# Kernel optimization log

Hardware: AMD Instinct MI355X
Metric: run time of the kernel (lower is better)

Reference implementation:

```python
import jax, jax.numpy as jnp
import numpy as np

N = 100000      # nodes
E = 800000      # directed edges
D_IN = 128      # input features (n_inputs)
HIDDEN = 128    # conf['model']['hidden_size']
D_OUT = 2       # conv2 output classes


def setup_inputs() -> dict:
    key = jax.random.key(0)
    k0, k1, k2, k3 = jax.random.split(key, 4)
    x = jax.random.normal(k0, (N, D_IN), dtype=jnp.float32)
    edge_index = jax.random.randint(k1, (2, E), 0, N, dtype=jnp.int32)
    # Glorot-style init for GCNConv weights, zero bias (PyG defaults)
    s1 = float(np.sqrt(6.0 / (D_IN + HIDDEN)))
    s2 = float(np.sqrt(6.0 / (HIDDEN + D_OUT)))
    W1 = jax.random.uniform(k2, (D_IN, HIDDEN), jnp.float32, -s1, s1)
    b1 = jnp.zeros((HIDDEN,), jnp.float32)
    W2 = jax.random.uniform(k3, (HIDDEN, D_OUT), jnp.float32, -s2, s2)
    b2 = jnp.zeros((D_OUT,), jnp.float32)
    return {"x": x, "edge_index": edge_index, "W1": W1, "b1": b1, "W2": W2, "b2": b2}


def gcn_conv(x, src, dst, W, b):
    """PyG GCNConv: add self-loops, symmetric deg^-1/2 A deg^-1/2 normalization."""
    n = x.shape[0]
    h = x @ W                                                   # [N, F_out]
    ones_e = jnp.ones((src.shape[0],), h.dtype)
    # degree with self-loops (init to 1)
    deg = jnp.ones((n,), h.dtype).at[dst].add(ones_e)           # [N]
    dinv = 1.0 / jnp.sqrt(deg)
    norm = (dinv[src] * dinv[dst])[:, None]                     # [E, 1]
    # self-loop contribution: norm_ii = dinv_i^2; then scatter edge messages
    out = (h * (dinv * dinv)[:, None]).at[dst].add(h[src] * norm)
    return out + b


def reference(x, edge_index, W1, b1, W2, b2):
    src, dst = edge_index[0], edge_index[1]
    h = jax.nn.relu(gcn_conv(x, src, dst, W1, b1))
    return gcn_conv(h, src, dst, W2, b2)                        # [N, 2]
```

## Files before the change

kernel.cpp:

```cpp
#include <hip/hip_runtime.h>
#include <hip/hip_bf16.h>


#define D1 128
#define BSH 8
#define BSZ (1 << BSH)
#define NBMAX 1024
#define CHA 2048
#define BMM 128

typedef __attribute__((ext_vector_type(8))) short short8;
typedef __attribute__((ext_vector_type(4))) float floatx4;

__device__ __forceinline__ unsigned short f2bf(float f) {
    unsigned u = __float_as_uint(f);
    u += 0x7fff + ((u >> 16) & 1);
    return (unsigned short)(u >> 16);
}
__device__ __forceinline__ float bflo(unsigned u) { return __uint_as_float(u << 16); }
__device__ __forceinline__ float bfhi(unsigned u) { return __uint_as_float(u & 0xffff0000u); }
__device__ __forceinline__ int clampN(int s, int N) {
    return (int)min((unsigned)s, (unsigned)N);
}

__global__ void k_init(const float* __restrict__ W1, unsigned short* __restrict__ W1t,
                       int* __restrict__ bcur, unsigned short* __restrict__ h1s,
                       float* __restrict__ h2s, float* __restrict__ dinv, int N) {
    int i = blockIdx.x * 256 + threadIdx.x;
    if (i < NBMAX) bcur[i] = 0;
    if (i < D1) h1s[(size_t)N * D1 + i] = 0;
    if (i < 2)  h2s[(size_t)N * 2 + i] = 0.f;
    if (i == 0) dinv[N] = 0.f;
    if (i < D1 * D1) {
        int c = i >> 7, k = i & 127;
        W1t[c * D1 + k] = f2bf(W1[k * D1 + c]);
    }
}

__global__ __launch_bounds__(512) void k_gemm1_binA(
    const float* __restrict__ x, const unsigned short* __restrict__ W1t,
    unsigned short* __restrict__ h1s,
    const int* __restrict__ src, const int* __restrict__ dst,
    int* __restrict__ bcur, unsigned* __restrict__ packed,
    int N, int E, int nbuck, int CAP, int GA, int GG)
{
    __shared__ __align__(16) char smem[2 * BMM * 136 * 2];

    const int b = blockIdx.x;
    const int m2 = 2 * min(GA, GG);
    bool isA;
    int bid;
    if (b < m2)            { isA = (b & 1); bid = b >> 1; }
    else if (GA <= GG)     { isA = false;   bid = min(GA, GG) + (b - m2); }
    else                   { isA = true;    bid = min(GA, GG) + (b - m2); }

    if (isA) {
        int* hist = (int*)smem;
        int* cur  = hist + NBMAX;
        const int t = threadIdx.x;
        const int e0 = bid * CHA;
        const int e1 = min(e0 + CHA, E);

        for (int i = t; i < nbuck; i += 512) hist[i] = 0;
        __syncthreads();
        for (int i = e0 + t; i < e1; i += 512)
            atomicAdd(&hist[dst[i] >> BSH], 1);
        __syncthreads();
        for (int i = t; i < nbuck; i += 512)
            cur[i] = (hist[i] > 0) ? atomicAdd(&bcur[i], hist[i]) : 0;
        __syncthreads();
        for (int i = e0 + t; i < e1; i += 512) {
            int d = dst[i];
            int bk = d >> BSH;
            int pos = atomicAdd(&cur[bk], 1);
            if (pos < CAP)
                packed[(size_t)bk * CAP + pos] =
                    ((unsigned)src[i] << BSH) | (unsigned)(d & (BSZ - 1));
        }
        return;
    }

    unsigned short (*Xs)[136] = (unsigned short(*)[136])smem;
    unsigned short (*Ws)[136] = (unsigned short(*)[136])(smem + BMM * 136 * 2);

    const int t = threadIdx.x;
    const int row0 = bid * BMM;

#pragma unroll
    for (int i = 0; i < 4; ++i) {
        int idx = t + 512 * i;
        int r = idx >> 4, c8 = idx & 15;
        short8 v = ((const short8*)W1t)[r * 16 + c8];
        *(short8*)&Ws[r][c8 * 8] = v;
    }
#pragma unroll
    for (int i = 0; i < 4; ++i) {
        int idx = t + 512 * i;
        int r = idx >> 4, c8 = idx & 15;
        int row = row0 + r;
        short8 v8 = (short8)0;
        if (row < N) {
            const float* p = x + (size_t)row * D1 + c8 * 8;
            float4 f0 = *(const float4*)p;
            float4 f1 = *(const float4*)(p + 4);
            v8[0] = (short)f2bf(f0.x); v8[1] = (short)f2bf(f0.y);
            v8[2] = (short)f2bf(f0.z); v8[3] = (short)f2bf(f0.w);
            v8[4] = (short)f2bf(f1.x); v8[5] = (short)f2bf(f1.y);
            v8[6] = (short)f2bf(f1.z); v8[7] = (short)f2bf(f1.w);
        }
        *(short8*)&Xs[r][c8 * 8] = v8;
    }
    __syncthreads();

    const int w = t >> 6;
    const int l = t & 63;
    const int m = l & 15;
    const int q = l >> 4;

    floatx4 acc[8];
#pragma unroll
    for (int c = 0; c < 8; ++c) acc[c] = (floatx4)0.0f;

#pragma unroll
    for (int ks = 0; ks < 4; ++ks) {
        short8 a = *(const short8*)&Xs[16 * w + m][ks * 32 + q * 8];
#pragma unroll
        for (int c = 0; c < 8; ++c) {
            short8 bb = *(const short8*)&Ws[c * 16 + m][ks * 32 + q * 8];
            acc[c] = __builtin_amdgcn_mfma_f32_16x16x32_bf16(a, bb, acc[c], 0, 0, 0);
        }
    }

    __syncthreads();

#pragma unroll
    for (int r = 0; r < 4; ++r) {
        int rt = 16 * w + q * 4 + r;
#pragma unroll
        for (int c = 0; c < 8; ++c)
            Xs[rt][c * 16 + m] = f2bf(acc[c][r]);
    }
    __syncthreads();

#pragma unroll
    for (int i = 0; i < 4; ++i) {
        int idx = t + 512 * i;
        int r = idx >> 4, c8 = idx & 15;
        int row = row0 + r;
        if (row < N)
            *(short8*)&h1s[(size_t)row * D1 + c8 * 8] = *(const short8*)&Xs[r][c8 * 8];
    }
}

__global__ __launch_bounds__(BSZ) void k_binB(
    const int* __restrict__ bcur, const unsigned* __restrict__ packed,
    int2* __restrict__ rp, float* __restrict__ dinv,
    int* __restrict__ esrc, int* __restrict__ order, int N, int CAP)
{
    __shared__ int lh[BSZ];
    __shared__ int lcur[BSZ];
    __shared__ int wsum[BSZ / 64];
    __shared__ int dbin[64];
    __shared__ int dcur[64];

    const int t = threadIdx.x;
    const int s = blockIdx.x << BSH;
    const int n = min(BSZ, N - s);
    const int base = blockIdx.x * CAP;
    const int cnt = min(bcur[blockIdx.x], CAP);

    lh[t] = 0;
    if (t < 64) dbin[t] = 0;
    __syncthreads();
    for (int i = t; i < cnt; i += BSZ)
        atomicAdd(&lh[packed[base + i] & (BSZ - 1)], 1);
    __syncthreads();

    const int deg = lh[t];
    const int pdeg = (deg + 3) & ~3;

    int inc = pdeg;
#pragma unroll
    for (int off = 1; off < 64; off <<= 1) {
        int u = __shfl_up(inc, off);
        if ((t & 63) >= off) inc += u;
    }
    if ((t & 63) == 63) wsum[t >> 6] = inc;
    __syncthreads();
    if (t < BSZ / 64) {
        int w = wsum[t];
#pragma unroll
        for (int off = 1; off < BSZ / 64; off <<= 1) {
            int u = __shfl_up(w, off, BSZ / 64);
            if ((t & (BSZ / 64 - 1)) >= off) w += u;
        }
        wsum[t] = w;
    }
    __syncthreads();
    int excl = ((t >> 6) ? wsum[(t >> 6) - 1] : 0) + inc - pdeg;

    if (t < n) {
        rp[s + t] = make_int2(base + excl, deg);
        dinv[s + t] = rsqrtf(1.0f + (float)deg);
        atomicAdd(&dbin[63 - min(deg, 63)], 1);
        for (int k = deg; k < pdeg; ++k) {
            int p = excl + k;
            if (p < CAP) esrc[base + p] = N;
        }
    }
    lcur[t] = excl;
    __syncthreads();

    for (int i = t; i < cnt; i += BSZ) {
        unsigned p = packed[base + i];
        int ld = (int)(p & (BSZ - 1));
        int pos = atomicAdd(&lcur[ld], 1);
        if (pos < CAP) esrc[base + pos] = (int)(p >> BSH);
    }

    __syncthreads();
    if (t < 64) {
        int dv = dbin[t];
        int dinc = dv;
#pragma unroll
        for (int off = 1; off < 64; off <<= 1) {
            int u = __shfl_up(dinc, off);
            if (t >= off) dinc += u;
        }
        dcur[t] = dinc - dv;
    }
    __syncthreads();
    if (t < n) {
        int b = 63 - min(deg, 63);
        int pos = atomicAdd(&dcur[b], 1);
        order[s + pos] = s + t;
    }
}

#define ACC8F(A, v, d) \
    A[0] += bflo(v.x) * d; A[1] += bfhi(v.x) * d; \
    A[2] += bflo(v.y) * d; A[3] += bfhi(v.y) * d; \
    A[4] += bflo(v.z) * d; A[5] += bfhi(v.z) * d; \
    A[6] += bflo(v.w) * d; A[7] += bfhi(v.w) * d;

__global__ __launch_bounds__(256) void k_agg1_gemm2(
    const int2* __restrict__ rp, const int* __restrict__ esrc,
    const int* __restrict__ order,
    const float* __restrict__ dinv, const unsigned short* __restrict__ h1s,
    const float* __restrict__ b1, const float* __restrict__ W2,
    float* __restrict__ h2s, int N)
{
    int gid = blockIdx.x * 256 + threadIdx.x;
    int grp = gid >> 4;
    if (grp >= N) return;
    int node = order[grp];
    int lane = gid & 15;

    const uint4* h1v = (const uint4*)h1s;
    const int4*  ev  = (const int4*)esrc;

    float di = dinv[node];
    uint4 u = h1v[(size_t)node * 16 + lane];
    float accA[8], accB[8];
    accA[0] = bflo(u.x) * di; accA[1] = bfhi(u.x) * di;
    accA[2] = bflo(u.y) * di; accA[3] = bfhi(u.y) * di;
    accA[4] = bflo(u.z) * di; accA[5] = bfhi(u.z) * di;
    accA[6] = bflo(u.w) * di; accA[7] = bfhi(u.w) * di;
#pragma unroll
    for (int j = 0; j < 8; ++j) accB[j] = 0.f;

    int2 r = rp[node];
    int beg = r.x;
    int end4 = beg + ((r.y + 3) & ~3);

    for (int e = beg; e < end4; e += 8) {
        int q = e >> 2;
        int4 i0 = ev[q];
        int4 i1 = ev[q + 1];
        bool c1 = (e + 4) < end4;
        int s0 = clampN(i0.x, N), s1 = clampN(i0.y, N);
        int s2 = clampN(i0.z, N), s3 = clampN(i0.w, N);
        int s4 = c1 ? clampN(i1.x, N) : N, s5 = c1 ? clampN(i1.y, N) : N;
        int s6 = c1 ? clampN(i1.z, N) : N, s7 = c1 ? clampN(i1.w, N) : N;
        float d0 = dinv[s0], d1 = dinv[s1], d2 = dinv[s2], d3 = dinv[s3];
        float d4 = dinv[s4], d5 = dinv[s5], d6 = dinv[s6], d7 = dinv[s7];
        uint4 v0 = h1v[(size_t)s0 * 16 + lane];
        uint4 v1 = h1v[(size_t)s1 * 16 + lane];
        uint4 v2 = h1v[(size_t)s2 * 16 + lane];
        uint4 v3 = h1v[(size_t)s3 * 16 + lane];
        uint4 v4 = h1v[(size_t)s4 * 16 + lane];
        uint4 v5 = h1v[(size_t)s5 * 16 + lane];
        uint4 v6 = h1v[(size_t)s6 * 16 + lane];
        uint4 v7 = h1v[(size_t)s7 * 16 + lane];
        ACC8F(accA, v0, d0) ACC8F(accB, v1, d1) ACC8F(accA, v2, d2) ACC8F(accB, v3, d3)
        ACC8F(accA, v4, d4) ACC8F(accB, v5, d5) ACC8F(accA, v6, d6) ACC8F(accB, v7, d7)
    }

    const float4* b1v = (const float4*)b1;
    float4 bbA = b1v[lane * 2 + 0];
    float4 bbB = b1v[lane * 2 + 1];
    float a[8];
    a[0] = fmaxf((accA[0] + accB[0]) * di + bbA.x, 0.f);
    a[1] = fmaxf((accA[1] + accB[1]) * di + bbA.y, 0.f);
    a[2] = fmaxf((accA[2] + accB[2]) * di + bbA.z, 0.f);
    a[3] = fmaxf((accA[3] + accB[3]) * di + bbA.w, 0.f);
    a[4] = fmaxf((accA[4] + accB[4]) * di + bbB.x, 0.f);
    a[5] = fmaxf((accA[5] + accB[5]) * di + bbB.y, 0.f);
    a[6] = fmaxf((accA[6] + accB[6]) * di + bbB.z, 0.f);
    a[7] = fmaxf((accA[7] + accB[7]) * di + bbB.w, 0.f);

    const float4* W2v = (const float4*)W2;
    float p0 = 0.f, p1 = 0.f;
#pragma unroll
    for (int j2 = 0; j2 < 4; ++j2) {
        float4 wv = W2v[lane * 4 + j2];
        p0 += a[j2 * 2] * wv.x + a[j2 * 2 + 1] * wv.z;
        p1 += a[j2 * 2] * wv.y + a[j2 * 2 + 1] * wv.w;
    }

#pragma unroll
    for (int off = 8; off > 0; off >>= 1) {
        p0 += __shfl_xor(p0, off);
        p1 += __shfl_xor(p1, off);
    }
    if (lane == 0) {
        h2s[(size_t)node * 2 + 0] = p0 * di;
        h2s[(size_t)node * 2 + 1] = p1 * di;
    }
}

__global__ void k_gather2(const int2* __restrict__ rp, const int* __restrict__ esrc,
                          const float* __restrict__ h2s, const float* __restrict__ dinv,
                          const float* __restrict__ b2, float* __restrict__ out, int N)
{
    int i = blockIdx.x * 256 + threadIdx.x;
    if (i >= N) return;
    const float2* h2v = (const float2*)h2s;
    const int4* ev = (const int4*)esrc;
    float2 h = h2v[i];
    float o0a = h.x, o1a = h.y;
    float o0b = 0.f, o1b = 0.f;
    int2 r = rp[i];
    int beg = r.x;
    int end4 = beg + ((r.y + 3) & ~3);
    for (int e = beg; e < end4; e += 16) {
        int q = e >> 2;
        int4 i0 = ev[q];
        int4 i1 = ev[q + 1];
        int4 i2 = ev[q + 2];
        int4 i3 = ev[q + 3];
        bool c1 = (e + 4) < end4, c2 = (e + 8) < end4, c3 = (e + 12) < end4;
        int s0 = clampN(i0.x, N), s1 = clampN(i0.y, N);
        int s2 = clampN(i0.z, N), s3 = clampN(i0.w, N);
        int s4 = c1 ? clampN(i1.x, N) : N, s5 = c1 ? clampN(i1.y, N) : N;
        int s6 = c1 ? clampN(i1.z, N) : N, s7 = c1 ? clampN(i1.w, N) : N;
        int s8 = c2 ? clampN(i2.x, N) : N, s9 = c2 ? clampN(i2.y, N) : N;
        int sa = c2 ? clampN(i2.z, N) : N, sb = c2 ? clampN(i2.w, N) : N;
        int sc = c3 ? clampN(i3.x, N) : N, sd = c3 ? clampN(i3.y, N) : N;
        int se = c3 ? clampN(i3.z, N) : N, sf = c3 ? clampN(i3.w, N) : N;
        float2 v0 = h2v[s0], v1 = h2v[s1], v2 = h2v[s2], v3 = h2v[s3];
        float2 v4 = h2v[s4], v5 = h2v[s5], v6 = h2v[s6], v7 = h2v[s7];
        float2 v8 = h2v[s8], v9 = h2v[s9], va = h2v[sa], vb = h2v[sb];
        float2 vc = h2v[sc], vd = h2v[sd], ve = h2v[se], vf = h2v[sf];
        o0a += v0.x + v2.x + v4.x + v6.x + v8.x + va.x + vc.x + ve.x;
        o1a += v0.y + v2.y + v4.y + v6.y + v8.y + va.y + vc.y + ve.y;
        o0b += v1.x + v3.x + v5.x + v7.x + v9.x + vb.x + vd.x + vf.x;
        o1b += v1.y + v3.y + v5.y + v7.y + v9.y + vb.y + vd.y + vf.y;
    }
    float di = dinv[i];
    ((float2*)out)[i] = make_float2((o0a + o0b) * di + b2[0], (o1a + o1b) * di + b2[1]);
}

extern "C" void kernel_launch(void* const* d_in, const int* in_sizes, int n_in,
                              void* d_out, int out_size, void* d_ws, size_t ws_size,
                              hipStream_t stream)
{
    const float* x  = (const float*)d_in[0];
    const int*   ei = (const int*)d_in[1];
    const float* W1 = (const float*)d_in[2];
    const float* b1 = (const float*)d_in[3];
    const float* W2 = (const float*)d_in[4];
    const float* b2 = (const float*)d_in[5];
    float* out = (float*)d_out;

    const int N = in_sizes[0] / D1;
    const int E = in_sizes[1] / 2;
    const int* src = ei;
    const int* dst = ei + E;

    const int nbuck = (N + BSZ - 1) >> BSH;
    const int avg = (E + nbuck - 1) / nbuck;
    const int CAP = (2 * avg + 3 * BSZ + 63) & ~63;

    char* w = (char*)d_ws;
    auto alloc = [&](size_t bytes) -> char* {
        char* r = w;
        w += (bytes + 63) & ~(size_t)63;
        return r;
    };
    unsigned short* h1s = (unsigned short*)alloc((size_t)(N + 1) * D1 * 2);
    unsigned short* W1t = (unsigned short*)alloc((size_t)D1 * D1 * 2);
    float* h2s    = (float*)alloc((size_t)(N + 1) * 2 * 4);
    float* dinv   = (float*)alloc((size_t)(N + 1) * 4);
    int2*  rp     = (int2*)alloc((size_t)N * 8);
    int*   order  = (int*)alloc((size_t)N * 4);
    int*   bcur   = (int*)alloc(NBMAX * 4);
    unsigned* packed = (unsigned*)alloc((size_t)nbuck * CAP * 4);
    int*   esrc   = (int*)alloc(((size_t)nbuck * CAP + 256) * 4);

    const int GA = (E + CHA - 1) / CHA;
    const int GG = (N + BMM - 1) / BMM;

    k_init <<<(D1 * D1 + 255) / 256, 256, 0, stream>>>(W1, W1t, bcur, h1s, h2s, dinv, N);
    k_gemm1_binA<<<GA + GG, 512, 0, stream>>>(x, W1t, h1s, src, dst, bcur, packed,
                                              N, E, nbuck, CAP, GA, GG);
    k_binB <<<nbuck, BSZ, 0, stream>>>(bcur, packed, rp, dinv, esrc, order, N, CAP);

    k_agg1_gemm2<<<(N * 16 + 255) / 256, 256, 0, stream>>>(rp, esrc, order, dinv, h1s, b1, W2, h2s, N);

    k_gather2<<<(N + 255) / 256, 256, 0, stream>>>(rp, esrc, h2s, dinv, b2, out, N);
}
```

Before: 179.8 us.

## Prescale GEMM1 rows by inverse sqrt degree to drop per-edge dinv gathers

A new pass in the init kernel counts node in-degrees with atomics. The GEMM1 epilogue uses those counts to multiply each row of h1 by rsqrt(1+deg) before rounding to bf16. The layer-1 aggregation then sums the pre-scaled neighbour rows and applies the destination dinv once, so it no longer gathers eight dinv values per edge step. The trade is an extra memset plus 800k global atomics on the critical path, and dinv[N] is no longer zeroed, which is a risk if later kernels read the padding entry.

Measured after the change: 205.9 us. 1.15x slower.

```diff
diff --git a/kernel.cpp b/kernel.cpp
--- a/kernel.cpp
+++ b/kernel.cpp
@@ -23,23 +23,26 @@
     return (int)min((unsigned)s, (unsigned)N);
 }
 
-__global__ void k_init(const float* __restrict__ W1, unsigned short* __restrict__ W1t,
-                       int* __restrict__ bcur, unsigned short* __restrict__ h1s,
-                       float* __restrict__ h2s, float* __restrict__ dinv, int N) {
+__global__ __launch_bounds__(256) void k_init(
+    const float* __restrict__ W1, unsigned short* __restrict__ W1t,
+    int* __restrict__ bcur, unsigned short* __restrict__ h1s,
+    float* __restrict__ h2s, const int* __restrict__ dst, int* __restrict__ deg,
+    int N, int E) {
     int i = blockIdx.x * 256 + threadIdx.x;
     if (i < NBMAX) bcur[i] = 0;
     if (i < D1) h1s[(size_t)N * D1 + i] = 0;
     if (i < 2)  h2s[(size_t)N * 2 + i] = 0.f;
-    if (i == 0) dinv[N] = 0.f;
     if (i < D1 * D1) {
         int c = i >> 7, k = i & 127;
         W1t[c * D1 + k] = f2bf(W1[k * D1 + c]);
     }
+    for (int e = i; e < E; e += gridDim.x * 256)
+        atomicAdd(&deg[dst[e]], 1);
 }
 
 __global__ __launch_bounds__(512) void k_gemm1_binA(
     const float* __restrict__ x, const unsigned short* __restrict__ W1t,
-    unsigned short* __restrict__ h1s,
+    const int* __restrict__ deg, unsigned short* __restrict__ h1s,
     const int* __restrict__ src, const int* __restrict__ dst,
     int* __restrict__ bcur, unsigned* __restrict__ packed,
     int N, int E, int nbuck, int CAP, int GA, int GG)
@@ -136,9 +139,11 @@
 #pragma unroll
     for (int r = 0; r < 4; ++r) {
         int rt = 16 * w + q * 4 + r;
+        int row = row0 + rt;
+        float di = (row < N) ? rsqrtf(1.0f + (float)deg[row]) : 0.f;
 #pragma unroll
         for (int c = 0; c < 8; ++c)
-            Xs[rt][c * 16 + m] = f2bf(acc[c][r]);
+            Xs[rt][c * 16 + m] = f2bf(acc[c][r] * di);
     }
     __syncthreads();
 
@@ -237,11 +242,11 @@
     }
 }
 
-#define ACC8F(A, v, d) \
-    A[0] += bflo(v.x) * d; A[1] += bfhi(v.x) * d; \
-    A[2] += bflo(v.y) * d; A[3] += bfhi(v.y) * d; \
-    A[4] += bflo(v.z) * d; A[5] += bfhi(v.z) * d; \
-    A[6] += bflo(v.w) * d; A[7] += bfhi(v.w) * d;
+#define ACC8(A, v) \
+    A[0] += bflo(v.x); A[1] += bfhi(v.x); \
+    A[2] += bflo(v.y); A[3] += bfhi(v.y); \
+    A[4] += bflo(v.z); A[5] += bfhi(v.z); \
+    A[6] += bflo(v.w); A[7] += bfhi(v.w);
 
 __global__ __launch_bounds__(256) void k_agg1_gemm2(
     const int2* __restrict__ rp, const int* __restrict__ esrc,
@@ -259,13 +264,12 @@
     const uint4* h1v = (const uint4*)h1s;
     const int4*  ev  = (const int4*)esrc;
 
-    float di = dinv[node];
     uint4 u = h1v[(size_t)node * 16 + lane];
     float accA[8], accB[8];
-    accA[0] = bflo(u.x) * di; accA[1] = bfhi(u.x) * di;
-    accA[2] = bflo(u.y) * di; accA[3] = bfhi(u.y) * di;
-    accA[4] = bflo(u.z) * di; accA[5] = bfhi(u.z) * di;
-    accA[6] = bflo(u.w) * di; accA[7] = bfhi(u.w) * di;
+    accA[0] = bflo(u.x); accA[1] = bfhi(u.x);
+    accA[2] = bflo(u.y); accA[3] = bfhi(u.y);
+    accA[4] = bflo(u.z); accA[5] = bfhi(u.z);
+    accA[6] = bflo(u.w); accA[7] = bfhi(u.w);
 #pragma unroll
     for (int j = 0; j < 8; ++j) accB[j] = 0.f;
 
@@ -282,8 +286,6 @@
         int s2 = clampN(i0.z, N), s3 = clampN(i0.w, N);
         int s4 = c1 ? clampN(i1.x, N) : N, s5 = c1 ? clampN(i1.y, N) : N;
         int s6 = c1 ? clampN(i1.z, N) : N, s7 = c1 ? clampN(i1.w, N) : N;
-        float d0 = dinv[s0], d1 = dinv[s1], d2 = dinv[s2], d3 = dinv[s3];
-        float d4 = dinv[s4], d5 = dinv[s5], d6 = dinv[s6], d7 = dinv[s7];
         uint4 v0 = h1v[(size_t)s0 * 16 + lane];
         uint4 v1 = h1v[(size_t)s1 * 16 + lane];
         uint4 v2 = h1v[(size_t)s2 * 16 + lane];
@@ -292,10 +294,11 @@
         uint4 v5 = h1v[(size_t)s5 * 16 + lane];
         uint4 v6 = h1v[(size_t)s6 * 16 + lane];
         uint4 v7 = h1v[(size_t)s7 * 16 + lane];
-        ACC8F(accA, v0, d0) ACC8F(accB, v1, d1) ACC8F(accA, v2, d2) ACC8F(accB, v3, d3)
-        ACC8F(accA, v4, d4) ACC8F(accB, v5, d5) ACC8F(accA, v6, d6) ACC8F(accB, v7, d7)
-    }
-
+        ACC8(accA, v0) ACC8(accB, v1) ACC8(accA, v2) ACC8(accB, v3)
+        ACC8(accA, v4) ACC8(accB, v5) ACC8(accA, v6) ACC8(accB, v7)
+    }
+
+    float di = dinv[node];
     const float4* b1v = (const float4*)b1;
     float4 bbA = b1v[lane * 2 + 0];
     float4 bbB = b1v[lane * 2 + 1];
@@ -402,6 +405,7 @@
     unsigned short* W1t = (unsigned short*)alloc((size_t)D1 * D1 * 2);
     float* h2s    = (float*)alloc((size_t)(N + 1) * 2 * 4);
     float* dinv   = (float*)alloc((size_t)(N + 1) * 4);
+    int*   deg    = (int*)alloc((size_t)N * 4);
     int2*  rp     = (int2*)alloc((size_t)N * 8);
     int*   order  = (int*)alloc((size_t)N * 4);
     int*   bcur   = (int*)alloc(NBMAX * 4);
@@ -411,8 +415,9 @@
     const int GA = (E + CHA - 1) / CHA;
     const int GG = (N + BMM - 1) / BMM;
 
-    k_init <<<(D1 * D1 + 255) / 256, 256, 0, stream>>>(W1, W1t, bcur, h1s, h2s, dinv, N);
-    k_gemm1_binA<<<GA + GG, 512, 0, stream>>>(x, W1t, h1s, src, dst, bcur, packed,
+    hipMemsetAsync(deg, 0, (size_t)N * 4, stream);
+    k_init <<<GA, 256, 0, stream>>>(W1, W1t, bcur, h1s, h2s, dst, deg, N, E);
+    k_gemm1_binA<<<GA + GG, 512, 0, stream>>>(x, W1t, deg, h1s, src, dst, bcur, packed,
                                               N, E, nbuck, CAP, GA, GG);
     k_binB <<<nbuck, BSZ, 0, stream>>>(bcur, packed, rp, dinv, esrc, order, N, CAP);
 
```
